# Kernel tuning notes

Hardware: AMD Instinct MI355X
Metric: run time of the kernel (lower is better)

Reference implementation:

```python
import jax, jax.numpy as jnp
import numpy as np

B, IN_DIM, H, L, P = 256, 64, 768, 4, 8
EPS = 1e-5


def _layernorm(h, g, b):
    mu = jnp.mean(h, axis=-1, keepdims=True)
    var = jnp.mean((h - mu) ** 2, axis=-1, keepdims=True)
    return (h - mu) * jax.lax.rsqrt(var + EPS) * g + b


def setup_inputs() -> dict:
    key = jax.random.key(0)
    ks = jax.random.split(key, 20)
    s_in = 1.0 / np.sqrt(IN_DIM)
    s_h = 1.0 / np.sqrt(H)
    return {
        "x": jax.random.normal(ks[0], (B, IN_DIM), jnp.float32),
        "w_in": jax.random.normal(ks[1], (IN_DIM, H), jnp.float32) * s_in,
        "b_in": jnp.zeros((H,), jnp.float32),
        "ln_g": jnp.ones((L, H), jnp.float32),
        "ln_b": jnp.zeros((L, H), jnp.float32),
        "trop_w": jax.random.normal(ks[2], (L, H, H), jnp.float32) * s_h,  # [L, out, in]
        "trop_b": jnp.zeros((L, H), jnp.float32),
        "lf_amax": jax.random.normal(ks[3], (L, H, P), jnp.float32) * 0.5 + 1.0,
        "lf_bmax": jax.random.normal(ks[4], (L, H, P), jnp.float32) * 0.1,
        "lf_amin": jax.random.normal(ks[5], (L, H, P), jnp.float32) * 0.5 + 1.0,
        "lf_bmin": jax.random.normal(ks[6], (L, H, P), jnp.float32) * 0.1,
        "lf_alpha": jnp.zeros((L, H), jnp.float32),
        "gate_w": jax.random.normal(ks[7], (L, H, H), jnp.float32) * 0.02,
        "gate_b": jnp.full((L, H), 2.0, jnp.float32),
        "cls_w": jax.random.normal(ks[8], (L, H, H), jnp.float32) * s_h,
        "cls_b": jnp.zeros((L, H), jnp.float32),
        "out_g": jnp.ones((H,), jnp.float32),
        "out_b": jnp.zeros((H,), jnp.float32),
        "head_w": jax.random.normal(ks[9], (H, 1), jnp.float32) * s_h,
        "head_b": jnp.zeros((1,), jnp.float32),
    }


def reference(x, w_in, b_in, ln_g, ln_b, trop_w, trop_b, lf_amax, lf_bmax,
              lf_amin, lf_bmin, lf_alpha, gate_w, gate_b, cls_w, cls_b,
              out_g, out_b, head_w, head_b):
    h = x @ w_in + b_in  # [B, H]
    for l in range(L):
        res = h
        hn = _layernorm(h, ln_g[l], ln_b[l])
        # Tropical (max-plus) linear: y[b,o] = max_i(hn[b,i] + W[o,i]) + bias[o]
        t = jnp.max(hn[:, None, :] + trop_w[l][None, :, :], axis=-1) + trop_b[l]
        # LF dual activation: blend of convex (max-plus) and concave (min-plus) PWL
        fmax = jnp.max(t[..., None] * lf_amax[l] + lf_bmax[l], axis=-1)  # [B, H]
        fmin = jnp.min(t[..., None] * lf_amin[l] + lf_bmin[l], axis=-1)
        a = jax.nn.sigmoid(lf_alpha[l])
        trop_out = a * fmax + (1.0 - a) * fmin
        class_out = jax.nn.gelu(hn @ cls_w[l] + cls_b[l], approximate=False)
        g = jax.nn.sigmoid(hn @ gate_w[l] + gate_b[l])
        h = res + g * trop_out + (1.0 - g) * class_out
    h = _layernorm(h, out_g, out_b)
    return (h @ head_w + head_b).squeeze(-1)  # [B]
```

## Files before the change

### kernel.cpp

```cpp
#include <hip/hip_runtime.h>
#include <math.h>

#define HDIM 768
#define BDIM 256
#define INDIM 64
#define NLAYERS 4
#define PDIM 8
#define KSPLIT 16
#define KLEN 48
#define CHK 16
#define TR 128
#define TC 64

__device__ __forceinline__ float sigmoidf_(float x) { return 1.f / (1.f + expf(-x)); }
__device__ __forceinline__ float geluf_(float x) { return 0.5f * x * (1.f + erff(x * 0.70710678118654752f)); }

__device__ __forceinline__ void gload_lds16(const float* g, float* l) {
    __builtin_amdgcn_global_load_lds((const __attribute__((address_space(1))) void*)g,
                                     (__attribute__((address_space(3))) void*)l, 16, 0, 0);
}

__global__ __launch_bounds__(256) void transpose_w_k(const float* __restrict__ src,
                                                     float* __restrict__ dst)
{
    __shared__ float tile[64][65];
    const int l = blockIdx.z;
    const int o0 = blockIdx.x * 64;
    const int i0 = blockIdx.y * 64;
    const int c = threadIdx.x & 63;
    const int r4 = threadIdx.x >> 6;
    const float* s = src + (size_t)l * HDIM * HDIM;
    float* d = dst + (size_t)l * HDIM * HDIM;
#pragma unroll
    for (int it = 0; it < 16; ++it) {
        const int r = it * 4 + r4;
        tile[r][c] = s[(size_t)(o0 + r) * HDIM + i0 + c];
    }
    __syncthreads();
#pragma unroll
    for (int it = 0; it < 16; ++it) {
        const int r = it * 4 + r4;
        d[(size_t)(i0 + r) * HDIM + o0 + c] = tile[c][r];
    }
}

__global__ __launch_bounds__(256) void input_ln_k(
    const float* __restrict__ x, const float* __restrict__ w_in,
    const float* __restrict__ b_in,
    const float* __restrict__ lng, const float* __restrict__ lnb,
    float* __restrict__ h, float* __restrict__ hnT)
{
    const int b = blockIdx.x;
    const int t = threadIdx.x;
    __shared__ float xs[INDIM];
    __shared__ float rbuf[8];
    if (t < INDIM) xs[t] = x[b * INDIM + t];
    __syncthreads();

    float acc0 = b_in[t], acc1 = b_in[t + 256], acc2 = b_in[t + 512];
#pragma unroll 8
    for (int i = 0; i < INDIM; ++i) {
        const float xv = xs[i];
        acc0 = fmaf(xv, w_in[i * HDIM + t], acc0);
        acc1 = fmaf(xv, w_in[i * HDIM + t + 256], acc1);
        acc2 = fmaf(xv, w_in[i * HDIM + t + 512], acc2);
    }
    h[(size_t)b * HDIM + t] = acc0;
    h[(size_t)b * HDIM + t + 256] = acc1;
    h[(size_t)b * HDIM + t + 512] = acc2;

    float s = acc0 + acc1 + acc2;
    float q = acc0 * acc0 + acc1 * acc1 + acc2 * acc2;
#pragma unroll
    for (int off = 32; off > 0; off >>= 1) { s += __shfl_down(s, off); q += __shfl_down(q, off); }
    const int wid = t >> 6, lane = t & 63;
    if (lane == 0) { rbuf[wid] = s; rbuf[4 + wid] = q; }
    __syncthreads();
    s = rbuf[0] + rbuf[1] + rbuf[2] + rbuf[3];
    q = rbuf[4] + rbuf[5] + rbuf[6] + rbuf[7];
    const float mu = s * (1.f / HDIM);
    const float var = q * (1.f / HDIM) - mu * mu;
    const float rsig = rsqrtf(var + 1e-5f);

    hnT[(size_t)(t)       * BDIM + b] = (acc0 - mu) * rsig * lng[t] + lnb[t];
    hnT[(size_t)(t + 256) * BDIM + b] = (acc1 - mu) * rsig * lng[t + 256] + lnb[t + 256];
    hnT[(size_t)(t + 512) * BDIM + b] = (acc2 - mu) * rsig * lng[t + 512] + lnb[t + 512];
}

__global__ __launch_bounds__(256, 2) void trop_mm_k(
    const float* __restrict__ hnT,
    const float* __restrict__ twT,
    float* __restrict__ p_trop)
{
    __shared__ float hn_s[2][CHK][TR];
    __shared__ float wt_s[2][CHK][TC];

    const int tid = threadIdx.x;
    const int sp = blockIdx.x;
    const int slot = blockIdx.y;
    const int col0 = (sp % 12) * TC;
    const int row0 = (sp / 12) * TR;
    const int k0 = slot * KLEN;

    const int wave = tid >> 6, lane = tid & 63;
    const int tx = tid & 15, ty = tid >> 4;
    const int r0 = ty * 8, c0 = tx * 4;

    const int hk = lane >> 5;
    const int hcol = (lane & 31) * 4;
    const int wr = lane >> 4;
    const int wcol = (lane & 15) * 4;

    float t_acc[8][4];
#pragma unroll
    for (int i = 0; i < 8; ++i)
#pragma unroll
        for (int j = 0; j < 4; ++j) t_acc[i][j] = -1e30f;

    #define STAGE_T(buf, kb)                                                                       \
    {                                                                                              \
        gload_lds16(hnT + (size_t)((kb) + 4 * wave + hk) * BDIM + row0 + hcol,                     \
                    &hn_s[buf][4 * wave][0]);                                                      \
        gload_lds16(hnT + (size_t)((kb) + 4 * wave + 2 + hk) * BDIM + row0 + hcol,                 \
                    &hn_s[buf][4 * wave + 2][0]);                                                  \
        gload_lds16(twT + (size_t)((kb) + 4 * wave + wr) * HDIM + col0 + wcol,                     \
                    &wt_s[buf][4 * wave][0]);                                                      \
    }

    STAGE_T(0, k0);
    __builtin_amdgcn_s_waitcnt(0);
    __syncthreads();

    for (int c = 0; c < KLEN / CHK; ++c) {
        const int buf = c & 1;
        if (c + 1 < KLEN / CHK) STAGE_T(1 - buf, k0 + (c + 1) * CHK);
#pragma unroll
        for (int k = 0; k < CHK; ++k) {
            const float4 h0 = *(const float4*)&hn_s[buf][k][r0];
            const float4 h1 = *(const float4*)&hn_s[buf][k][r0 + 4];
            const float4 wt = *(const float4*)&wt_s[buf][k][c0];
            const float hf[8] = {h0.x, h0.y, h0.z, h0.w, h1.x, h1.y, h1.z, h1.w};
            const float wtf[4] = {wt.x, wt.y, wt.z, wt.w};
#pragma unroll
            for (int i = 0; i < 8; ++i)
#pragma unroll
                for (int j = 0; j < 4; ++j)
                    t_acc[i][j] = fmaxf(t_acc[i][j], hf[i] + wtf[j]);
        }
        __builtin_amdgcn_s_waitcnt(0);
        __syncthreads();
    }
    #undef STAGE_T

    const size_t base = (size_t)slot * BDIM * HDIM;
#pragma unroll
    for (int i = 0; i < 8; ++i) {
        const size_t off = base + (size_t)(row0 + r0 + i) * HDIM + col0 + c0;
        *(float4*)(p_trop + off) = make_float4(t_acc[i][0], t_acc[i][1], t_acc[i][2], t_acc[i][3]);
    }
}

__global__ __launch_bounds__(256, 2) void cg_mm_k(
    const float* __restrict__ hnT,
    const float* __restrict__ cwp,
    const float* __restrict__ gwp,
    float* __restrict__ p_cls, float* __restrict__ p_gate)
{
    __shared__ float hn_s[2][CHK][TR];
    __shared__ float wc_s[2][CHK][TC];
    __shared__ float wg_s[2][CHK][TC];

    const int tid = threadIdx.x;
    const int sp = blockIdx.x;
    const int slot = blockIdx.y;
    const int col0 = (sp % 12) * TC;
    const int row0 = (sp / 12) * TR;
    const int k0 = slot * KLEN;

    const int wave = tid >> 6, lane = tid & 63;
    const int tx = tid & 15, ty = tid >> 4;
    const int r0 = ty * 8, c0 = tx * 4;

    const int hk = lane >> 5;
    const int hcol = (lane & 31) * 4;
    const int wr = lane >> 4;
    const int wcol = (lane & 15) * 4;

    float c_acc[8][4], g_acc[8][4];
#pragma unroll
    for (int i = 0; i < 8; ++i)
#pragma unroll
        for (int j = 0; j < 4; ++j) { c_acc[i][j] = 0.f; g_acc[i][j] = 0.f; }

    #define STAGE_CG(buf, kb)                                                                      \
    {                                                                                              \
        gload_lds16(hnT + (size_t)((kb) + 4 * wave + hk) * BDIM + row0 + hcol,                     \
                    &hn_s[buf][4 * wave][0]);                                                      \
        gload_lds16(hnT + (size_t)((kb) + 4 * wave + 2 + hk) * BDIM + row0 + hcol,                 \
                    &hn_s[buf][4 * wave + 2][0]);                                                  \
        gload_lds16(cwp + (size_t)((kb) + 4 * wave + wr) * HDIM + col0 + wcol,                     \
                    &wc_s[buf][4 * wave][0]);                                                      \
        gload_lds16(gwp + (size_t)((kb) + 4 * wave + wr) * HDIM + col0 + wcol,                     \
                    &wg_s[buf][4 * wave][0]);                                                      \
    }

    STAGE_CG(0, k0);
    __builtin_amdgcn_s_waitcnt(0);
    __syncthreads();

    for (int c = 0; c < KLEN / CHK; ++c) {
        const int buf = c & 1;
        if (c + 1 < KLEN / CHK) STAGE_CG(1 - buf, k0 + (c + 1) * CHK);
#pragma unroll
        for (int k = 0; k < CHK; ++k) {
            const float4 h0 = *(const float4*)&hn_s[buf][k][r0];
            const float4 h1 = *(const float4*)&hn_s[buf][k][r0 + 4];
            const float4 wc = *(const float4*)&wc_s[buf][k][c0];
            const float4 wg = *(const float4*)&wg_s[buf][k][c0];
            const float hf[8] = {h0.x, h0.y, h0.z, h0.w, h1.x, h1.y, h1.z, h1.w};
            const float wcf[4] = {wc.x, wc.y, wc.z, wc.w};
            const float wgf[4] = {wg.x, wg.y, wg.z, wg.w};
#pragma unroll
            for (int i = 0; i < 8; ++i)
#pragma unroll
                for (int j = 0; j < 4; ++j) {
                    c_acc[i][j] = fmaf(hf[i], wcf[j], c_acc[i][j]);
                    g_acc[i][j] = fmaf(hf[i], wgf[j], g_acc[i][j]);
                }
        }
        __builtin_amdgcn_s_waitcnt(0);
        __syncthreads();
    }
    #undef STAGE_CG

    const size_t base = (size_t)slot * BDIM * HDIM;
#pragma unroll
    for (int i = 0; i < 8; ++i) {
        const size_t off = base + (size_t)(row0 + r0 + i) * HDIM + col0 + c0;
        *(float4*)(p_cls + off)  = make_float4(c_acc[i][0], c_acc[i][1], c_acc[i][2], c_acc[i][3]);
        *(float4*)(p_gate + off) = make_float4(g_acc[i][0], g_acc[i][1], g_acc[i][2], g_acc[i][3]);
    }
}

__global__ __launch_bounds__(768) void combine_k(
    const float* __restrict__ p_trop, const float* __restrict__ p_cls, const float* __restrict__ p_gate,
    const float* __restrict__ trop_b,
    const float* __restrict__ amax, const float* __restrict__ bmax,
    const float* __restrict__ amin, const float* __restrict__ bmin,
    const float* __restrict__ alpha,
    const float* __restrict__ gate_b, const float* __restrict__ cls_b,
    float* __restrict__ h,
    const float* __restrict__ lng, const float* __restrict__ lnb,
    float* __restrict__ hnT,
    const float* __restrict__ head_w, const float* __restrict__ head_b,
    float* __restrict__ out, const int is_last)
{
    const int b = blockIdx.x;
    const int o = threadIdx.x;
    __shared__ float rbuf[12], qbuf[12];

    const size_t base = (size_t)b * HDIM + o;
    float tm = -1e30f, cs = 0.f, gs = 0.f;
#pragma unroll
    for (int k = 0; k < KSPLIT; ++k) {
        const size_t idx = (size_t)k * BDIM * HDIM + base;
        tm = fmaxf(tm, p_trop[idx]);
        cs += p_cls[idx];
        gs += p_gate[idx];
    }
    const float tv = tm + trop_b[o];
    float fmx = -1e30f, fmn = 1e30f;
#pragma unroll
    for (int p = 0; p < PDIM; ++p) {
        fmx = fmaxf(fmx, fmaf(tv, amax[o * PDIM + p], bmax[o * PDIM + p]));
        fmn = fminf(fmn, fmaf(tv, amin[o * PDIM + p], bmin[o * PDIM + p]));
    }
    const float a = sigmoidf_(alpha[o]);
    const float trop_out = a * fmx + (1.f - a) * fmn;
    const float cls_out = geluf_(cs + cls_b[o]);
    const float g = sigmoidf_(gs + gate_b[o]);
    const float val = h[base] + g * trop_out + (1.f - g) * cls_out;
    h[base] = val;

    float s = val, q = val * val;
#pragma unroll
    for (int off = 32; off > 0; off >>= 1) { s += __shfl_down(s, off); q += __shfl_down(q, off); }
    const int wid = o >> 6, lane = o & 63;
    if (lane == 0) { rbuf[wid] = s; qbuf[wid] = q; }
    __syncthreads();
    s = 0.f; q = 0.f;
#pragma unroll
    for (int w = 0; w < 12; ++w) { s += rbuf[w]; q += qbuf[w]; }
    const float mu = s * (1.f / HDIM);
    const float var = q * (1.f / HDIM) - mu * mu;
    const float rsig = rsqrtf(var + 1e-5f);
    const float ln_v = (val - mu) * rsig * lng[o] + lnb[o];

    if (!is_last) {
        hnT[(size_t)o * BDIM + b] = ln_v;
    } else {
        float part = ln_v * head_w[o];
#pragma unroll
        for (int off = 32; off > 0; off >>= 1) part += __shfl_down(part, off);
        __syncthreads();
        if (lane == 0) rbuf[wid] = part;
        __syncthreads();
        if (o == 0) {
            float r = head_b[0];
#pragma unroll
            for (int w = 0; w < 12; ++w) r += rbuf[w];
            out[b] = r;
        }
    }
}

extern "C" void kernel_launch(void* const* d_in, const int* in_sizes, int n_in,
                              void* d_out, int out_size, void* d_ws, size_t ws_size,
                              hipStream_t stream)
{
    const float* x       = (const float*)d_in[0];
    const float* w_in    = (const float*)d_in[1];
    const float* b_in    = (const float*)d_in[2];
    const float* ln_g    = (const float*)d_in[3];
    const float* ln_b    = (const float*)d_in[4];
    const float* trop_w  = (const float*)d_in[5];
    const float* trop_b  = (const float*)d_in[6];
    const float* lf_amax = (const float*)d_in[7];
    const float* lf_bmax = (const float*)d_in[8];
    const float* lf_amin = (const float*)d_in[9];
    const float* lf_bmin = (const float*)d_in[10];
    const float* lf_alpha= (const float*)d_in[11];
    const float* gate_w  = (const float*)d_in[12];
    const float* gate_b  = (const float*)d_in[13];
    const float* cls_w   = (const float*)d_in[14];
    const float* cls_b   = (const float*)d_in[15];
    const float* out_g   = (const float*)d_in[16];
    const float* out_b   = (const float*)d_in[17];
    const float* head_w  = (const float*)d_in[18];
    const float* head_b  = (const float*)d_in[19];
    float* out = (float*)d_out;

    const size_t NBH = (size_t)BDIM * HDIM;
    const size_t WSZ = (size_t)HDIM * HDIM;
    float* ws = (float*)d_ws;
    float* h      = ws;
    float* hnT    = ws + NBH;
    float* twT    = ws + 2 * NBH;
    float* p_trop = twT + (size_t)NLAYERS * WSZ;
    float* p_cls  = p_trop + (size_t)KSPLIT * NBH;
    float* p_gate = p_cls + (size_t)KSPLIT * NBH;

    transpose_w_k<<<dim3(12, 12, NLAYERS), 256, 0, stream>>>(trop_w, twT);
    input_ln_k<<<BDIM, 256, 0, stream>>>(x, w_in, b_in, ln_g, ln_b, h, hnT);

    for (int l = 0; l < NLAYERS; ++l) {
        trop_mm_k<<<dim3(24, KSPLIT), 256, 0, stream>>>(
            hnT, twT + (size_t)l * WSZ, p_trop);
        cg_mm_k<<<dim3(24, KSPLIT), 256, 0, stream>>>(
            hnT, cls_w + (size_t)l * WSZ, gate_w + (size_t)l * WSZ, p_cls, p_gate);

        const int is_last = (l == NLAYERS - 1);
        combine_k<<<BDIM, 768, 0, stream>>>(
            p_trop, p_cls, p_gate,
            trop_b + (size_t)l * HDIM,
            lf_amax + (size_t)l * HDIM * PDIM, lf_bmax + (size_t)l * HDIM * PDIM,
            lf_amin + (size_t)l * HDIM * PDIM, lf_bmin + (size_t)l * HDIM * PDIM,
            lf_alpha + (size_t)l * HDIM,
            gate_b + (size_t)l * HDIM, cls_b + (size_t)l * HDIM,
            h,
            is_last ? out_g : ln_g + (size_t)(l + 1) * HDIM,
            is_last ? out_b : ln_b + (size_t)(l + 1) * HDIM,
            hnT, head_w, head_b, out, is_last);
    }
}
```

Before: 257.1 us.

## Compute cls/gate matmuls with bf16 MFMA instead of fp32 split-K FMA

Replaces the fp32 split-K SIMT matmul for the classic and gate branches with a bf16 MFMA kernel that runs the full K dimension per block. Weights are transposed and converted to bf16 once per call, and activations are also written in bf16 row-major form by the LN kernels. This removes the KSPLIT partial-sum buffers and their reduction in combine, at the cost of bf16 precision and loading operands directly from global memory without LDS staging.

```diff
diff --git a/kernel.cpp b/kernel.cpp
--- a/kernel.cpp
+++ b/kernel.cpp
@@ -12,8 +12,16 @@
 #define TR 128
 #define TC 64
 
+typedef short bf16x8 __attribute__((ext_vector_type(8)));
+typedef float f32x4 __attribute__((ext_vector_type(4)));
+
 __device__ __forceinline__ float sigmoidf_(float x) { return 1.f / (1.f + expf(-x)); }
 __device__ __forceinline__ float geluf_(float x) { return 0.5f * x * (1.f + erff(x * 0.70710678118654752f)); }
+__device__ __forceinline__ unsigned short f2bf(float f) {
+    unsigned int u = __float_as_uint(f);
+    u += 0x7FFFu + ((u >> 16) & 1u);
+    return (unsigned short)(u >> 16);
+}
 
 __device__ __forceinline__ void gload_lds16(const float* g, float* l) {
     __builtin_amdgcn_global_load_lds((const __attribute__((address_space(1))) void*)g,
@@ -44,11 +52,37 @@
     }
 }
 
+__global__ __launch_bounds__(256) void wprep_k(const float* __restrict__ cls_w,
+                                               const float* __restrict__ gate_w,
+                                               unsigned short* __restrict__ wB)
+{
+    __shared__ float tile[64][65];
+    const int z = blockIdx.z;
+    const int l = z >> 1, mat = z & 1;
+    const int o0 = blockIdx.x * 64;
+    const int k0 = blockIdx.y * 64;
+    const int c = threadIdx.x & 63;
+    const int r4 = threadIdx.x >> 6;
+    const float* s = (mat ? gate_w : cls_w) + (size_t)l * HDIM * HDIM;
+    unsigned short* d = wB + (size_t)z * HDIM * HDIM;
+#pragma unroll
+    for (int it = 0; it < 16; ++it) {
+        const int r = it * 4 + r4;
+        tile[r][c] = s[(size_t)(k0 + r) * HDIM + o0 + c];
+    }
+    __syncthreads();
+#pragma unroll
+    for (int it = 0; it < 16; ++it) {
+        const int r = it * 4 + r4;
+        d[(size_t)(o0 + r) * HDIM + k0 + c] = f2bf(tile[c][r]);
+    }
+}
+
 __global__ __launch_bounds__(256) void input_ln_k(
     const float* __restrict__ x, const float* __restrict__ w_in,
     const float* __restrict__ b_in,
     const float* __restrict__ lng, const float* __restrict__ lnb,
-    float* __restrict__ h, float* __restrict__ hnT)
+    float* __restrict__ h, float* __restrict__ hnT, unsigned short* __restrict__ hnB)
 {
     const int b = blockIdx.x;
     const int t = threadIdx.x;
@@ -82,9 +116,14 @@
     const float var = q * (1.f / HDIM) - mu * mu;
     const float rsig = rsqrtf(var + 1e-5f);
 
-    hnT[(size_t)(t)       * BDIM + b] = (acc0 - mu) * rsig * lng[t] + lnb[t];
-    hnT[(size_t)(t + 256) * BDIM + b] = (acc1 - mu) * rsig * lng[t + 256] + lnb[t + 256];
-    hnT[(size_t)(t + 512) * BDIM + b] = (acc2 - mu) * rsig * lng[t + 512] + lnb[t + 512];
+#pragma unroll
+    for (int qq = 0; qq < 3; ++qq) {
+        const int o = t + qq * 256;
+        const float av = (qq == 0) ? acc0 : (qq == 1) ? acc1 : acc2;
+        const float v = (av - mu) * rsig * lng[o] + lnb[o];
+        hnT[(size_t)o * BDIM + b] = v;
+        hnB[(size_t)b * HDIM + o] = f2bf(v);
+    }
 }
 
 __global__ __launch_bounds__(256, 2) void trop_mm_k(
@@ -160,86 +199,48 @@
     }
 }
 
-__global__ __launch_bounds__(256, 2) void cg_mm_k(
-    const float* __restrict__ hnT,
-    const float* __restrict__ cwp,
-    const float* __restrict__ gwp,
+__global__ __launch_bounds__(256, 4) void cg_mfma_k(
+    const unsigned short* __restrict__ hnB,
+    const unsigned short* __restrict__ wB,
     float* __restrict__ p_cls, float* __restrict__ p_gate)
 {
-    __shared__ float hn_s[2][CHK][TR];
-    __shared__ float wc_s[2][CHK][TC];
-    __shared__ float wg_s[2][CHK][TC];
-
-    const int tid = threadIdx.x;
-    const int sp = blockIdx.x;
-    const int slot = blockIdx.y;
-    const int col0 = (sp % 12) * TC;
-    const int row0 = (sp / 12) * TR;
-    const int k0 = slot * KLEN;
-
-    const int wave = tid >> 6, lane = tid & 63;
-    const int tx = tid & 15, ty = tid >> 4;
-    const int r0 = ty * 8, c0 = tx * 4;
-
-    const int hk = lane >> 5;
-    const int hcol = (lane & 31) * 4;
-    const int wr = lane >> 4;
-    const int wcol = (lane & 15) * 4;
-
-    float c_acc[8][4], g_acc[8][4];
-#pragma unroll
-    for (int i = 0; i < 8; ++i)
-#pragma unroll
-        for (int j = 0; j < 4; ++j) { c_acc[i][j] = 0.f; g_acc[i][j] = 0.f; }
-
-    #define STAGE_CG(buf, kb)                                                                      \
-    {                                                                                              \
-        gload_lds16(hnT + (size_t)((kb) + 4 * wave + hk) * BDIM + row0 + hcol,                     \
-                    &hn_s[buf][4 * wave][0]);                                                      \
-        gload_lds16(hnT + (size_t)((kb) + 4 * wave + 2 + hk) * BDIM + row0 + hcol,                 \
-                    &hn_s[buf][4 * wave + 2][0]);                                                  \
-        gload_lds16(cwp + (size_t)((kb) + 4 * wave + wr) * HDIM + col0 + wcol,                     \
-                    &wc_s[buf][4 * wave][0]);                                                      \
-        gload_lds16(gwp + (size_t)((kb) + 4 * wave + wr) * HDIM + col0 + wcol,                     \
-                    &wg_s[buf][4 * wave][0]);                                                      \
-    }
-
-    STAGE_CG(0, k0);
-    __builtin_amdgcn_s_waitcnt(0);
-    __syncthreads();
-
-    for (int c = 0; c < KLEN / CHK; ++c) {
-        const int buf = c & 1;
-        if (c + 1 < KLEN / CHK) STAGE_CG(1 - buf, k0 + (c + 1) * CHK);
-#pragma unroll
-        for (int k = 0; k < CHK; ++k) {
-            const float4 h0 = *(const float4*)&hn_s[buf][k][r0];
-            const float4 h1 = *(const float4*)&hn_s[buf][k][r0 + 4];
-            const float4 wc = *(const float4*)&wc_s[buf][k][c0];
-            const float4 wg = *(const float4*)&wg_s[buf][k][c0];
-            const float hf[8] = {h0.x, h0.y, h0.z, h0.w, h1.x, h1.y, h1.z, h1.w};
-            const float wcf[4] = {wc.x, wc.y, wc.z, wc.w};
-            const float wgf[4] = {wg.x, wg.y, wg.z, wg.w};
-#pragma unroll
-            for (int i = 0; i < 8; ++i)
-#pragma unroll
-                for (int j = 0; j < 4; ++j) {
-                    c_acc[i][j] = fmaf(hf[i], wcf[j], c_acc[i][j]);
-                    g_acc[i][j] = fmaf(hf[i], wgf[j], g_acc[i][j]);
-                }
+    const int wave = threadIdx.x >> 6, lane = threadIdx.x & 63;
+    const int m0 = blockIdx.x * 64 + wave * 16;
+    const int n0 = blockIdx.y * 64;
+    const int lm = lane & 15;
+    const int q  = lane >> 4;
+
+    const unsigned short* wc = wB;
+    const unsigned short* wg = wB + (size_t)HDIM * HDIM;
+
+    f32x4 acc[2][4];
+#pragma unroll
+    for (int m = 0; m < 2; ++m)
+#pragma unroll
+        for (int nn = 0; nn < 4; ++nn) acc[m][nn] = (f32x4){0.f, 0.f, 0.f, 0.f};
+
+    const unsigned short* aptr = hnB + (size_t)(m0 + lm) * HDIM + q * 8;
+#pragma unroll 2
+    for (int k0 = 0; k0 < HDIM; k0 += 32) {
+        const bf16x8 a = *(const bf16x8*)(aptr + k0);
+#pragma unroll
+        for (int nn = 0; nn < 4; ++nn) {
+            const size_t woff = (size_t)(n0 + nn * 16 + lm) * HDIM + k0 + q * 8;
+            const bf16x8 bc = *(const bf16x8*)(wc + woff);
+            const bf16x8 bg = *(const bf16x8*)(wg + woff);
+            acc[0][nn] = __builtin_amdgcn_mfma_f32_16x16x32_bf16(a, bc, acc[0][nn], 0, 0, 0);
+            acc[1][nn] = __builtin_amdgcn_mfma_f32_16x16x32_bf16(a, bg, acc[1][nn], 0, 0, 0);
         }
-        __builtin_amdgcn_s_waitcnt(0);
-        __syncthreads();
-    }
-    #undef STAGE_CG
-
-    const size_t base = (size_t)slot * BDIM * HDIM;
-#pragma unroll
-    for (int i = 0; i < 8; ++i) {
-        const size_t off = base + (size_t)(row0 + r0 + i) * HDIM + col0 + c0;
-        *(float4*)(p_cls + off)  = make_float4(c_acc[i][0], c_acc[i][1], c_acc[i][2], c_acc[i][3]);
-        *(float4*)(p_gate + off) = make_float4(g_acc[i][0], g_acc[i][1], g_acc[i][2], g_acc[i][3]);
-    }
+    }
+
+#pragma unroll
+    for (int nn = 0; nn < 4; ++nn)
+#pragma unroll
+        for (int r = 0; r < 4; ++r) {
+            const size_t off = (size_t)(m0 + q * 4 + r) * HDIM + n0 + nn * 16 + lm;
+            p_cls[off]  = acc[0][nn][r];
+            p_gate[off] = acc[1][nn][r];
+        }
 }
 
 __global__ __launch_bounds__(768) void combine_k(
@@ -251,7 +252,7 @@
     const float* __restrict__ gate_b, const float* __restrict__ cls_b,
     float* __restrict__ h,
     const float* __restrict__ lng, const float* __restrict__ lnb,
-    float* __restrict__ hnT,
+    float* __restrict__ hnT, unsigned short* __restrict__ hnB,
     const float* __restrict__ head_w, const float* __restrict__ head_b,
     float* __restrict__ out, const int is_last)
 {
@@ -260,14 +261,13 @@
     __shared__ float rbuf[12], qbuf[12];
 
     const size_t base = (size_t)b * HDIM + o;
-    float tm = -1e30f, cs = 0.f, gs = 0.f;
-#pragma unroll
-    for (int k = 0; k < KSPLIT; ++k) {
-        const size_t idx = (size_t)k * BDIM * HDIM + base;
-        tm = fmaxf(tm, p_trop[idx]);
-        cs += p_cls[idx];
-        gs += p_gate[idx];
-    }
+    float tm = -1e30f;
+#pragma unroll
+    for (int k = 0; k < KSPLIT; ++k)
+        tm = fmaxf(tm, p_trop[(size_t)k * BDIM * HDIM + base]);
+    const float cs = p_cls[base];
+    const float gs = p_gate[base];
+
     const float tv = tm + trop_b[o];
     float fmx = -1e30f, fmn = 1e30f;
 #pragma unroll
@@ -298,6 +298,7 @@
 
     if (!is_last) {
         hnT[(size_t)o * BDIM + b] = ln_v;
+        hnB[base] = f2bf(ln_v);
     } else {
         float part = ln_v * head_w[o];
 #pragma unroll
@@ -348,16 +349,19 @@
     float* twT    = ws + 2 * NBH;
     float* p_trop = twT + (size_t)NLAYERS * WSZ;
     float* p_cls  = p_trop + (size_t)KSPLIT * NBH;
-    float* p_gate = p_cls + (size_t)KSPLIT * NBH;
+    float* p_gate = p_cls + NBH;
+    unsigned short* hnB = (unsigned short*)(p_gate + NBH);
+    unsigned short* wB  = hnB + NBH;
 
     transpose_w_k<<<dim3(12, 12, NLAYERS), 256, 0, stream>>>(trop_w, twT);
-    input_ln_k<<<BDIM, 256, 0, stream>>>(x, w_in, b_in, ln_g, ln_b, h, hnT);
+    wprep_k<<<dim3(12, 12, 2 * NLAYERS), 256, 0, stream>>>(cls_w, gate_w, wB);
+    input_ln_k<<<BDIM, 256, 0, stream>>>(x, w_in, b_in, ln_g, ln_b, h, hnT, hnB);
 
     for (int l = 0; l < NLAYERS; ++l) {
         trop_mm_k<<<dim3(24, KSPLIT), 256, 0, stream>>>(
             hnT, twT + (size_t)l * WSZ, p_trop);
-        cg_mm_k<<<dim3(24, KSPLIT), 256, 0, stream>>>(
-            hnT, cls_w + (size_t)l * WSZ, gate_w + (size_t)l * WSZ, p_cls, p_gate);
+        cg_mfma_k<<<dim3(4, 12), 256, 0, stream>>>(
+            hnB, wB + (size_t)(2 * l) * WSZ, p_cls, p_gate);
 
         const int is_last = (l == NLAYERS - 1);
         combine_k<<<BDIM, 768, 0, stream>>>(
@@ -370,6 +374,6 @@
             h,
             is_last ? out_g : ln_g + (size_t)(l + 1) * HDIM,
             is_last ? out_b : ln_b + (size_t)(l + 1) * HDIM,
-            hnT, head_w, head_b, out, is_last);
-    }
-}
+            hnT, hnB, head_w, head_b, out, is_last);
+    }
+}
```

After: 332.3 us. 29.2% more time.
